# Performance work log

Measured on AMD Instinct MI355X. Metric: run time of the kernel, lower is better.

## Reference

```python
import jax, jax.numpy as jnp
import numpy as np
from jax import lax

C = 64      # mid_channels
CR = 16     # reduced channels (C // reduction_ratio 4)
G = 4       # groups (C // group_channels 16)
K = 7       # involution kernel size
L = 6       # number of involution layers (n_layers - 2)
EPS = 1e-5
DN = ('NCHW', 'OIHW', 'NCHW')


def conv3(x, w, b):
    # 3x3 conv, stride 1, no padding (torch Conv2d default)
    y = lax.conv_general_dilated(x, w, (1, 1), [(0, 0), (0, 0)], dimension_numbers=DN)
    return y + b[None, :, None, None]


def conv1x1(x, w, b):
    # pointwise conv as einsum over channels
    return jnp.einsum('oi,bihw->bohw', w, x) + b[None, :, None, None]


def involution(x, wr, br, g, bt, mu, var, ws, bs):
    B, Cc, H, W = x.shape
    # kernel generation: 1x1 reduce -> BN (eval) -> ReLU -> 1x1 span
    t = conv1x1(x, wr, br)
    t = (t - mu[None, :, None, None]) * (g * jax.lax.rsqrt(var + EPS))[None, :, None, None] + bt[None, :, None, None]
    t = jax.nn.relu(t)
    w = conv1x1(t, ws, bs)                    # (B, G*K*K, H, W)
    w = w.reshape(B, G, K * K, H, W)
    # unfold: patches ordered (C, Kh, Kw) along channel dim, matching torch unfold
    p = lax.conv_general_dilated_patches(x, (K, K), (1, 1), [(K // 2, K // 2)] * 2, dimension_numbers=DN)
    p = p.reshape(B, G, Cc // G, K * K, H, W)
    out = jnp.einsum('bgkhw,bgckhw->bgchw', w, p)
    return out.reshape(B, Cc, H, W)


def setup_inputs() -> dict:
    key = jax.random.key(0)
    ks = jax.random.split(key, 9)
    s = 0.05
    return {
        'input_tensor': jax.random.normal(ks[0], (1, 3, 128, 128), jnp.float32),
        'conv_in_w': jax.random.normal(ks[1], (C, 3, 3, 3), jnp.float32) * s,
        'conv_in_b': jax.random.normal(ks[2], (C,), jnp.float32) * s,
        'w_reduce': jax.random.normal(ks[3], (L, CR, C), jnp.float32) * s,
        'b_reduce': jax.random.normal(ks[4], (L, CR), jnp.float32) * s,
        'bn_gamma': jnp.ones((L, CR), jnp.float32),
        'bn_beta': jnp.zeros((L, CR), jnp.float32),
        'bn_mean': jnp.zeros((L, CR), jnp.float32),
        'bn_var': jnp.ones((L, CR), jnp.float32),
        'w_span': jax.random.normal(ks[5], (L, G * K * K, CR), jnp.float32) * s,
        'b_span': jax.random.normal(ks[6], (L, G * K * K), jnp.float32) * s,
        'conv_out_w': jax.random.normal(ks[7], (2 * C, C, 3, 3), jnp.float32) * s,
        'conv_out_b': jax.random.normal(ks[8], (2 * C,), jnp.float32) * s,
    }


def reference(input_tensor, conv_in_w, conv_in_b, w_reduce, b_reduce, bn_gamma,
              bn_beta, bn_mean, bn_var, w_span, b_span, conv_out_w, conv_out_b):
    x = conv3(input_tensor, conv_in_w, conv_in_b)          # (1, 64, 126, 126)
    for i in range(L):
        x = jax.nn.relu(involution(x, w_reduce[i], b_reduce[i], bn_gamma[i],
                                   bn_beta[i], bn_mean[i], bn_var[i],
                                   w_span[i], b_span[i]))
    return conv3(x, conv_out_w, conv_out_b)                # (1, 128, 124, 124)
```

## Files before the change

kernel.cpp:

```cpp
#include <hip/hip_runtime.h>

#define IH 126
#define IW 126
#define HW 15876
#define OH 124
#define OW 124
#define OHW 15376

__global__ __launch_bounds__(256) void conv_in_kernel(
    const float* __restrict__ x, const float* __restrict__ w,
    const float* __restrict__ b, float* __restrict__ y)
{
  int pix = blockIdx.x * 256 + threadIdx.x;
  if (pix >= HW) return;
  int oc = blockIdx.y;
  int h  = pix / IW;
  int wc = pix - h * IW;
  const float* wp = w + oc * 27;
  float acc = b[oc];
#pragma unroll
  for (int ci = 0; ci < 3; ci++)
#pragma unroll
    for (int ky = 0; ky < 3; ky++)
#pragma unroll
      for (int kx = 0; kx < 3; kx++)
        acc = fmaf(x[ci * 128 * 128 + (h + ky) * 128 + (wc + kx)],
                   wp[ci * 9 + ky * 3 + kx], acc);
  y[oc * HW + pix] = acc;
}

__global__ __launch_bounds__(512, 4) void inv_kernel(
    const float* __restrict__ x, float* __restrict__ y,
    const float* __restrict__ wr, const float* __restrict__ br,
    const float* __restrict__ gam, const float* __restrict__ bet,
    const float* __restrict__ mu, const float* __restrict__ var,
    const float* __restrict__ wspan, const float* __restrict__ bspan)
{
  __shared__ __align__(16) float xs[140][68];
  __shared__ __align__(16) float wvs[6272];
  float* tss = &wvs[5632];
  float* ob  = &xs[0][0];

  int tid = threadIdx.x;
  int bx = blockIdx.x & 15, by = blockIdx.x >> 4;
  int ox0 = bx * 8, oy0 = by * 4;
  int xh0 = ox0 - 3, yh0 = oy0 - 3;

  for (int idx = tid; idx < 140 * 64; idx += 512) {
    int c = idx / 140;
    int pos = idx - c * 140;
    int row = pos / 14;
    int col = pos - row * 14;
    int gy = yh0 + row, gx = xh0 + col;
    float v = 0.f;
    if (gy >= 0 && gy < IH && gx >= 0 && gx < IW)
      v = x[c * HW + gy * IW + gx];
    xs[pos][c] = v;
  }
  __syncthreads();

  int w_ = __builtin_amdgcn_readfirstlane(tid >> 6);
  int ln = tid & 63;
  int p  = ln & 31;
  int prow = p >> 3, pcol = p & 7;
  int pc = (prow + 3) * 14 + (pcol + 3);

  {
    int cr0 = 2 * w_;
    const float* wa = wr + cr0 * 64;
    const float* wb = wa + 64;
    float a0 = 0.f, a1 = 0.f;
#pragma unroll
    for (int ci = 0; ci < 64; ci += 4) {
      float4 xv = *(const float4*)&xs[pc][ci];
      a0 = fmaf(xv.x, wa[ci + 0], a0); a1 = fmaf(xv.x, wb[ci + 0], a1);
      a0 = fmaf(xv.y, wa[ci + 1], a0); a1 = fmaf(xv.y, wb[ci + 1], a1);
      a0 = fmaf(xv.z, wa[ci + 2], a0); a1 = fmaf(xv.z, wb[ci + 2], a1);
      a0 = fmaf(xv.w, wa[ci + 3], a0); a1 = fmaf(xv.w, wb[ci + 3], a1);
    }
    float s0 = gam[cr0]     * rsqrtf(var[cr0]     + 1e-5f);
    float s1 = gam[cr0 + 1] * rsqrtf(var[cr0 + 1] + 1e-5f);
    float t0 = (a0 + br[cr0]     - mu[cr0])     * s0 + bet[cr0];
    float t1 = (a1 + br[cr0 + 1] - mu[cr0 + 1]) * s1 + bet[cr0 + 1];
    if (ln < 32) {
      tss[p * 20 + cr0]     = fmaxf(t0, 0.f);
      tss[p * 20 + cr0 + 1] = fmaxf(t1, 0.f);
    }
  }
  __syncthreads();

  {
    float tv[16];
#pragma unroll
    for (int i = 0; i < 4; i++) {
      float4 t4 = *(const float4*)&tss[p * 20 + 4 * i];
      tv[4 * i] = t4.x; tv[4 * i + 1] = t4.y;
      tv[4 * i + 2] = t4.z; tv[4 * i + 3] = t4.w;
    }
    __syncthreads();
    for (int j = 0; j < 25; j++) {
      int pair = w_ + 8 * j;
      if (pair < 196) {
        const float* wk = wspan + pair * 16;
        float a = bspan[pair];
#pragma unroll
        for (int i = 0; i < 16; i++) a = fmaf(tv[i], wk[i], a);
        if (ln < 32) wvs[pair * 32 + pcol * 4 + prow] = a;
      }
    }
  }
  __syncthreads();

  float acc0 = 0.f, acc1 = 0.f, acc2 = 0.f, acc3 = 0.f;
  {
    int c = ln;
    int g = ln >> 4;
    float xw[4][7];
#pragma unroll
    for (int r = 0; r < 4; r++)
#pragma unroll
      for (int kx = 0; kx < 7; kx++)
        xw[r][kx] = xs[r * 14 + w_ + kx][c];
#pragma unroll
    for (int ky = 0; ky < 7; ky++) {
      if (ky > 0) {
#pragma unroll
        for (int r = 0; r < 3; r++)
#pragma unroll
          for (int kx = 0; kx < 7; kx++) xw[r][kx] = xw[r + 1][kx];
#pragma unroll
        for (int kx = 0; kx < 7; kx++)
          xw[3][kx] = xs[(ky + 3) * 14 + w_ + kx][c];
      }
#pragma unroll
      for (int kx = 0; kx < 7; kx++) {
        int k = ky * 7 + kx;
        float4 w4 = *(const float4*)&wvs[(g * 49 + k) * 32 + w_ * 4];
        acc0 = fmaf(w4.x, xw[0][kx], acc0);
        acc1 = fmaf(w4.y, xw[1][kx], acc1);
        acc2 = fmaf(w4.z, xw[2][kx], acc2);
        acc3 = fmaf(w4.w, xw[3][kx], acc3);
      }
    }
  }
  __syncthreads();

  {
    int c = ln;
    ob[c * 33 + 0 * 8 + w_] = fmaxf(acc0, 0.f);
    ob[c * 33 + 1 * 8 + w_] = fmaxf(acc1, 0.f);
    ob[c * 33 + 2 * 8 + w_] = fmaxf(acc2, 0.f);
    ob[c * 33 + 3 * 8 + w_] = fmaxf(acc3, 0.f);
  }
  __syncthreads();
  for (int j = tid; j < 2048; j += 512) {
    int c2 = j >> 5, pp = j & 31;
    int pr = pp >> 3, pc2 = pp & 7;
    int gy = oy0 + pr, gx = ox0 + pc2;
    if (gy < IH && gx < IW)
      y[c2 * HW + gy * IW + gx] = ob[c2 * 33 + pp];
  }
}

__global__ __launch_bounds__(256) void transpose_w_kernel(
    const float* __restrict__ w, float* __restrict__ wt)
{
  int i = blockIdx.x * 256 + threadIdx.x;
  if (i >= 128 * 64 * 9) return;
  int oc = i / 576;
  int rem = i - oc * 576;
  int ci = rem / 9;
  int k = rem - ci * 9;
  wt[(k * 64 + ci) * 128 + oc] = w[i];
}

__global__ __launch_bounds__(256, 6) void conv_out_kernel(
    const float* __restrict__ x, const float* __restrict__ wt,
    const float* __restrict__ b, float* __restrict__ y)
{
  __shared__ __align__(16) float xsm[16 * 100 * 4];
  int tid = threadIdx.x;
  int bx = blockIdx.x & 15, by = blockIdx.x >> 4;
  int oy0 = by * 8, ox0 = bx * 8;

  for (int u = tid; u < 1600; u += 256) {
    int cq = u / 100;
    int pos = u - cq * 100;
    int row = pos / 10;
    int col = pos - row * 10;
    int gy = oy0 + row, gx = ox0 + col;
    float4 v = make_float4(0.f, 0.f, 0.f, 0.f);
    if (gy < IH && gx < IW) {
      const float* xp = x + cq * 4 * HW + gy * IW + gx;
      v.x = xp[0]; v.y = xp[HW]; v.z = xp[2 * HW]; v.w = xp[3 * HW];
    }
    *(float4*)&xsm[u * 4] = v;
  }
  __syncthreads();

  int ln = tid & 63;
  int px = ln & 7, py = ln >> 3;
  int wv_ = __builtin_amdgcn_readfirstlane(tid >> 6);
  int oc8 = blockIdx.y * 32 + wv_ * 8;

  float acc[8];
#pragma unroll
  for (int j = 0; j < 8; j++) acc[j] = b[oc8 + j];

#pragma unroll
  for (int ky = 0; ky < 3; ky++) {
#pragma unroll
    for (int kx = 0; kx < 3; kx++) {
      int k = ky * 3 + kx;
      int pidx = (py + ky) * 10 + px + kx;
      const float* wp = wt + k * 64 * 128 + oc8;
#pragma unroll 4
      for (int cq = 0; cq < 16; cq++) {
        float4 xv = *(const float4*)&xsm[(cq * 100 + pidx) * 4];
        const float* wq = wp + cq * 4 * 128;
#pragma unroll
        for (int j = 0; j < 8; j++) {
          acc[j] = fmaf(xv.x, wq[0 * 128 + j], acc[j]);
          acc[j] = fmaf(xv.y, wq[1 * 128 + j], acc[j]);
          acc[j] = fmaf(xv.z, wq[2 * 128 + j], acc[j]);
          acc[j] = fmaf(xv.w, wq[3 * 128 + j], acc[j]);
        }
      }
    }
  }

  int oy = oy0 + py, ox = ox0 + px;
  if (oy < OH && ox < OW) {
#pragma unroll
    for (int j = 0; j < 8; j++)
      y[(oc8 + j) * OHW + oy * OW + ox] = acc[j];
  }
}

extern "C" void kernel_launch(void* const* d_in, const int* in_sizes, int n_in,
                              void* d_out, int out_size, void* d_ws, size_t ws_size,
                              hipStream_t stream)
{
  const float* input = (const float*)d_in[0];
  const float* ciw   = (const float*)d_in[1];
  const float* cib   = (const float*)d_in[2];
  const float* wred  = (const float*)d_in[3];
  const float* bred  = (const float*)d_in[4];
  const float* gam   = (const float*)d_in[5];
  const float* bet   = (const float*)d_in[6];
  const float* mu    = (const float*)d_in[7];
  const float* var   = (const float*)d_in[8];
  const float* wspan = (const float*)d_in[9];
  const float* bspan = (const float*)d_in[10];
  const float* cow   = (const float*)d_in[11];
  const float* cob   = (const float*)d_in[12];
  float* out = (float*)d_out;

  float* bufA = (float*)d_ws;
  float* bufB = bufA + (1 << 20);
  float* wt   = bufA + (1 << 21);

  transpose_w_kernel<<<288, 256, 0, stream>>>(cow, wt);
  conv_in_kernel<<<dim3(63, 64), 256, 0, stream>>>(input, ciw, cib, bufA);

  float* cur = bufA; float* nxt = bufB;
  for (int i = 0; i < 6; i++) {
    inv_kernel<<<512, 512, 0, stream>>>(cur, nxt,
        wred + i * 16 * 64, bred + i * 16, gam + i * 16, bet + i * 16,
        mu + i * 16, var + i * 16, wspan + i * 196 * 16, bspan + i * 196);
    float* t = cur; cur = nxt; nxt = t;
  }
  conv_out_kernel<<<dim3(256, 4), 256, 0, stream>>>(cur, wt, cob, out);
}
```

Before: 254.2 us.

## Split involution into weight-generation and einsum kernels over padded activation planes

Replaces the fused per-tile involution kernel with two kernels per layer. A wgen kernel computes the per-pixel 196-entry kernel field into global memory, and an einsum kernel applies it row by row. Activations are stored in zero-padded 136x132 planes, which removes the bounds checks and the shared-memory halo staging. The per-layer weight field (about 12 MB) now round-trips through global memory, wgen runs only 249 blocks while holding 64 input values per thread in registers, and the kernel launch count doubles.

```diff
diff --git a/kernel.cpp b/kernel.cpp
--- a/kernel.cpp
+++ b/kernel.cpp
@@ -6,6 +6,18 @@
 #define OH 124
 #define OW 124
 #define OHW 15376
+
+#define PR 136
+#define PROWS 132
+#define PLANE (PR * PROWS)
+
+__global__ __launch_bounds__(256) void zero_kernel(float* __restrict__ p, int n4)
+{
+  int i = blockIdx.x * 256 + threadIdx.x;
+  int stride = gridDim.x * 256;
+  for (; i < n4; i += stride)
+    *(float4*)&p[4 * i] = make_float4(0.f, 0.f, 0.f, 0.f);
+}
 
 __global__ __launch_bounds__(256) void conv_in_kernel(
     const float* __restrict__ x, const float* __restrict__ w,
@@ -26,140 +38,88 @@
       for (int kx = 0; kx < 3; kx++)
         acc = fmaf(x[ci * 128 * 128 + (h + ky) * 128 + (wc + kx)],
                    wp[ci * 9 + ky * 3 + kx], acc);
-  y[oc * HW + pix] = acc;
-}
-
-__global__ __launch_bounds__(512, 4) void inv_kernel(
-    const float* __restrict__ x, float* __restrict__ y,
+  y[oc * PLANE + (h + 3) * PR + (wc + 3)] = acc;
+}
+
+__global__ __launch_bounds__(256) void wgen_kernel(
+    const float* __restrict__ x, float* __restrict__ wf,
     const float* __restrict__ wr, const float* __restrict__ br,
     const float* __restrict__ gam, const float* __restrict__ bet,
     const float* __restrict__ mu, const float* __restrict__ var,
     const float* __restrict__ wspan, const float* __restrict__ bspan)
 {
-  __shared__ __align__(16) float xs[140][68];
-  __shared__ __align__(16) float wvs[6272];
-  float* tss = &wvs[5632];
-  float* ob  = &xs[0][0];
-
   int tid = threadIdx.x;
-  int bx = blockIdx.x & 15, by = blockIdx.x >> 4;
-  int ox0 = bx * 8, oy0 = by * 4;
-  int xh0 = ox0 - 3, yh0 = oy0 - 3;
-
-  for (int idx = tid; idx < 140 * 64; idx += 512) {
-    int c = idx / 140;
-    int pos = idx - c * 140;
-    int row = pos / 14;
-    int col = pos - row * 14;
-    int gy = yh0 + row, gx = xh0 + col;
-    float v = 0.f;
-    if (gy >= 0 && gy < IH && gx >= 0 && gx < IW)
-      v = x[c * HW + gy * IW + gx];
-    xs[pos][c] = v;
-  }
-  __syncthreads();
-
-  int w_ = __builtin_amdgcn_readfirstlane(tid >> 6);
   int ln = tid & 63;
-  int p  = ln & 31;
-  int prow = p >> 3, pcol = p & 7;
-  int pc = (prow + 3) * 14 + (pcol + 3);
-
-  {
-    int cr0 = 2 * w_;
-    const float* wa = wr + cr0 * 64;
-    const float* wb = wa + 64;
-    float a0 = 0.f, a1 = 0.f;
-#pragma unroll
-    for (int ci = 0; ci < 64; ci += 4) {
-      float4 xv = *(const float4*)&xs[pc][ci];
-      a0 = fmaf(xv.x, wa[ci + 0], a0); a1 = fmaf(xv.x, wb[ci + 0], a1);
-      a0 = fmaf(xv.y, wa[ci + 1], a0); a1 = fmaf(xv.y, wb[ci + 1], a1);
-      a0 = fmaf(xv.z, wa[ci + 2], a0); a1 = fmaf(xv.z, wb[ci + 2], a1);
-      a0 = fmaf(xv.w, wa[ci + 3], a0); a1 = fmaf(xv.w, wb[ci + 3], a1);
-    }
-    float s0 = gam[cr0]     * rsqrtf(var[cr0]     + 1e-5f);
-    float s1 = gam[cr0 + 1] * rsqrtf(var[cr0 + 1] + 1e-5f);
-    float t0 = (a0 + br[cr0]     - mu[cr0])     * s0 + bet[cr0];
-    float t1 = (a1 + br[cr0 + 1] - mu[cr0 + 1]) * s1 + bet[cr0 + 1];
-    if (ln < 32) {
-      tss[p * 20 + cr0]     = fmaxf(t0, 0.f);
-      tss[p * 20 + cr0 + 1] = fmaxf(t1, 0.f);
-    }
-  }
-  __syncthreads();
-
-  {
-    float tv[16];
-#pragma unroll
-    for (int i = 0; i < 4; i++) {
-      float4 t4 = *(const float4*)&tss[p * 20 + 4 * i];
-      tv[4 * i] = t4.x; tv[4 * i + 1] = t4.y;
-      tv[4 * i + 2] = t4.z; tv[4 * i + 3] = t4.w;
-    }
-    __syncthreads();
-    for (int j = 0; j < 25; j++) {
-      int pair = w_ + 8 * j;
-      if (pair < 196) {
-        const float* wk = wspan + pair * 16;
-        float a = bspan[pair];
-#pragma unroll
-        for (int i = 0; i < 16; i++) a = fmaf(tv[i], wk[i], a);
-        if (ln < 32) wvs[pair * 32 + pcol * 4 + prow] = a;
-      }
-    }
-  }
-  __syncthreads();
-
-  float acc0 = 0.f, acc1 = 0.f, acc2 = 0.f, acc3 = 0.f;
-  {
-    int c = ln;
-    int g = ln >> 4;
-    float xw[4][7];
-#pragma unroll
-    for (int r = 0; r < 4; r++)
-#pragma unroll
-      for (int kx = 0; kx < 7; kx++)
-        xw[r][kx] = xs[r * 14 + w_ + kx][c];
-#pragma unroll
-    for (int ky = 0; ky < 7; ky++) {
-      if (ky > 0) {
-#pragma unroll
-        for (int r = 0; r < 3; r++)
-#pragma unroll
-          for (int kx = 0; kx < 7; kx++) xw[r][kx] = xw[r + 1][kx];
-#pragma unroll
-        for (int kx = 0; kx < 7; kx++)
-          xw[3][kx] = xs[(ky + 3) * 14 + w_ + kx][c];
-      }
-#pragma unroll
-      for (int kx = 0; kx < 7; kx++) {
-        int k = ky * 7 + kx;
-        float4 w4 = *(const float4*)&wvs[(g * 49 + k) * 32 + w_ * 4];
-        acc0 = fmaf(w4.x, xw[0][kx], acc0);
-        acc1 = fmaf(w4.y, xw[1][kx], acc1);
-        acc2 = fmaf(w4.z, xw[2][kx], acc2);
-        acc3 = fmaf(w4.w, xw[3][kx], acc3);
-      }
-    }
-  }
-  __syncthreads();
-
-  {
-    int c = ln;
-    ob[c * 33 + 0 * 8 + w_] = fmaxf(acc0, 0.f);
-    ob[c * 33 + 1 * 8 + w_] = fmaxf(acc1, 0.f);
-    ob[c * 33 + 2 * 8 + w_] = fmaxf(acc2, 0.f);
-    ob[c * 33 + 3 * 8 + w_] = fmaxf(acc3, 0.f);
-  }
-  __syncthreads();
-  for (int j = tid; j < 2048; j += 512) {
-    int c2 = j >> 5, pp = j & 31;
-    int pr = pp >> 3, pc2 = pp & 7;
-    int gy = oy0 + pr, gx = ox0 + pc2;
-    if (gy < IH && gx < IW)
-      y[c2 * HW + gy * IW + gx] = ob[c2 * 33 + pp];
-  }
+  int q = __builtin_amdgcn_readfirstlane(tid >> 6);
+  int p = blockIdx.x * 64 + ln;
+  int py = p / 126;
+  int px = p - py * 126;
+  const float* xp = x + (py + 3) * PR + (px + 3);
+
+  float xv[64];
+#pragma unroll
+  for (int ci = 0; ci < 64; ci++) xv[ci] = xp[ci * PLANE];
+
+  float t[16];
+#pragma unroll
+  for (int j = 0; j < 16; j++) {
+    const float* wrow = wr + j * 64;
+    float a = 0.f;
+#pragma unroll
+    for (int ci = 0; ci < 64; ci++) a = fmaf(xv[ci], wrow[ci], a);
+    float s = gam[j] * rsqrtf(var[j] + 1e-5f);
+    t[j] = fmaxf((a + br[j] - mu[j]) * s + bet[j], 0.f);
+  }
+
+  bool ok = (p < HW);
+  const float* wsb = wspan + q * 49 * 16;
+  const float* bsb = bspan + q * 49;
+  float* out = wf + q * 49 * HW + p;
+  for (int jj = 0; jj < 49; jj++) {
+    const float* wk = wsb + jj * 16;
+    float a = bsb[jj];
+#pragma unroll
+    for (int i = 0; i < 16; i++) a = fmaf(t[i], wk[i], a);
+    if (ok) out[jj * HW] = a;
+  }
+}
+
+__global__ __launch_bounds__(256) void einsum_kernel(
+    const float* __restrict__ x, const float* __restrict__ wf,
+    float* __restrict__ y)
+{
+  int tid = threadIdx.x;
+  int ln = tid & 63;
+  int wv = __builtin_amdgcn_readfirstlane(tid >> 6);
+  int row = blockIdx.x;
+  int ch = blockIdx.y * 4 + wv;
+  int g = ch >> 4;
+  if (ln >= 63) return;
+  int x0 = 2 * ln;
+
+  const float* xpl = x + ch * PLANE;
+  const float* wbase = wf + g * 49 * HW + row * 126 + x0;
+  float a0 = 0.f, a1 = 0.f;
+#pragma unroll
+  for (int ky = 0; ky < 7; ky++) {
+    const float* xr = xpl + (row + ky) * PR + x0;
+    float xv[8];
+#pragma unroll
+    for (int h = 0; h < 4; h++) {
+      float2 v = *(const float2*)(xr + 2 * h);
+      xv[2 * h] = v.x; xv[2 * h + 1] = v.y;
+    }
+    const float* wr_ = wbase + ky * 7 * HW;
+#pragma unroll
+    for (int kx = 0; kx < 7; kx++) {
+      float2 w2 = *(const float2*)(wr_ + kx * HW);
+      a0 = fmaf(w2.x, xv[kx], a0);
+      a1 = fmaf(w2.y, xv[kx + 1], a1);
+    }
+  }
+  float* yp = y + ch * PLANE + (row + 3) * PR + (x0 + 3);
+  yp[0] = fmaxf(a0, 0.f);
+  yp[1] = fmaxf(a1, 0.f);
 }
 
 __global__ __launch_bounds__(256) void transpose_w_kernel(
@@ -191,8 +151,8 @@
     int gy = oy0 + row, gx = ox0 + col;
     float4 v = make_float4(0.f, 0.f, 0.f, 0.f);
     if (gy < IH && gx < IW) {
-      const float* xp = x + cq * 4 * HW + gy * IW + gx;
-      v.x = xp[0]; v.y = xp[HW]; v.z = xp[2 * HW]; v.w = xp[3 * HW];
+      const float* xp = x + cq * 4 * PLANE + (gy + 3) * PR + (gx + 3);
+      v.x = xp[0]; v.y = xp[PLANE]; v.z = xp[2 * PLANE]; v.w = xp[3 * PLANE];
     }
     *(float4*)&xsm[u * 4] = v;
   }
@@ -256,18 +216,22 @@
   const float* cob   = (const float*)d_in[12];
   float* out = (float*)d_out;
 
-  float* bufA = (float*)d_ws;
-  float* bufB = bufA + (1 << 20);
-  float* wt   = bufA + (1 << 21);
-
+  float* ws = (float*)d_ws;
+  float* bufA   = ws;
+  float* bufB   = ws + 1200000;
+  float* wfield = ws + 2400000;
+  float* wt     = ws + 5600000;
+
+  zero_kernel<<<1024, 256, 0, stream>>>(ws, 600000);
   transpose_w_kernel<<<288, 256, 0, stream>>>(cow, wt);
   conv_in_kernel<<<dim3(63, 64), 256, 0, stream>>>(input, ciw, cib, bufA);
 
   float* cur = bufA; float* nxt = bufB;
   for (int i = 0; i < 6; i++) {
-    inv_kernel<<<512, 512, 0, stream>>>(cur, nxt,
+    wgen_kernel<<<249, 256, 0, stream>>>(cur, wfield,
         wred + i * 16 * 64, bred + i * 16, gam + i * 16, bet + i * 16,
         mu + i * 16, var + i * 16, wspan + i * 196 * 16, bspan + i * 196);
+    einsum_kernel<<<dim3(126, 16), 256, 0, stream>>>(cur, wfield, nxt);
     float* t = cur; cur = nxt; nxt = t;
   }
   conv_out_kernel<<<dim3(256, 4), 256, 0, stream>>>(cur, wt, cob, out);
```

Result: slower. 435.7 us (+71.4%).
